# Performance work log

Measured on AMD Instinct MI355X. Metric: run time of the kernel, lower is better.

Reference implementation:

```python
import jax, jax.numpy as jnp
import numpy as np
import math

SUB_LEN = 5

def _row_mask(index, sub_len, win_len):
    # Faithful port of logsparseAttention.row_mask (numpy, built at trace time).
    log_l = math.ceil(math.log2(sub_len))
    mask = np.zeros(win_len, dtype=np.float32)
    if (win_len // sub_len) * 2 * log_l > index:
        mask[: index + 1] = 1.0
    else:
        while index >= 0:
            if index - log_l + 1 < 0:
                mask[:index] = 1.0
                break
            mask[index - log_l + 1 : index + 1] = 1.0
            for i in range(log_l):
                new_index = index - log_l + 1 - 2 ** i
                if index - new_index <= sub_len and new_index >= 0:
                    mask[new_index] = 1.0
            index -= sub_len
    return mask

def _log_mask(win_len, sub_len):
    m = np.stack([_row_mask(i, sub_len, win_len) for i in range(win_len)])
    return m[None, None]  # [1, 1, L, L]

def setup_inputs() -> dict:
    key = jax.random.key(0)
    kq, kk, kv = jax.random.split(key, 3)
    B, L, H, D = 4, 2048, 16, 64
    return {
        "queries": jax.random.normal(kq, (B, L, H, D), dtype=jnp.float32),
        "keys": jax.random.normal(kk, (B, L, H, D), dtype=jnp.float32),
        "values": jax.random.normal(kv, (B, L, H, D), dtype=jnp.float32),
        "attn_mask": jnp.zeros((1,), dtype=jnp.int32),  # unused by the module
    }

def reference(queries, keys, values, attn_mask):
    L = queries.shape[1]
    mask = jnp.asarray(_log_mask(L, SUB_LEN), dtype=queries.dtype)  # [1,1,L,L]
    q = jnp.swapaxes(queries, 1, 2)            # [B, H, L, D]
    k = jnp.transpose(keys, (0, 2, 3, 1))      # [B, H, D, L]
    v = jnp.swapaxes(values, 1, 2)             # [B, H, L, D]
    pre_att = jnp.matmul(q, k)                 # [B, H, L, L] (no scaling: scale=None)
    pre_att = pre_att * mask + (-1e9) * (1.0 - mask)
    att = jax.nn.softmax(pre_att, axis=-1)
    return jnp.matmul(att, v)                  # [B, H, L, D]
```

## Files before the change

### kernel.cpp

```cpp
#include <hip/hip_runtime.h>


typedef __attribute__((ext_vector_type(8))) short short8;
typedef __attribute__((ext_vector_type(4))) float floatx4;
typedef __attribute__((ext_vector_type(16))) float floatx16;
typedef _Float16 half8 __attribute__((ext_vector_type(8)));
typedef _Float16 half4 __attribute__((ext_vector_type(4)));
typedef unsigned int uint32_t4 __attribute__((ext_vector_type(4)));

#define NB 4
#define NL 2048
#define NH 16
#define ND 64
#define PADK 72
#define LOG2E 1.44269504088896340736f

#define KSW(row, col8) (((row) << 6) + ((col8) ^ (((row) & 7) << 3)))

static __device__ __forceinline__ unsigned short f2bf(float f) {
    unsigned int u = __float_as_uint(f);
    u += 0x7fff + ((u >> 16) & 1);
    return (unsigned short)(u >> 16);
}
static __device__ __forceinline__ float bf2f(unsigned short h) {
    return __uint_as_float(((unsigned int)h) << 16);
}
static __device__ __forceinline__ floatx16 fzero16() {
    floatx16 z;
    #pragma unroll
    for (int i = 0; i < 16; ++i) z[i] = 0.f;
    return z;
}

static __device__ __forceinline__ void plswap2(unsigned int& a, unsigned int& b, int hi) {
#if __has_builtin(__builtin_amdgcn_permlane32_swap)
    auto r = __builtin_amdgcn_permlane32_swap(a, b, false, false);
    a = (unsigned int)r[0];
    b = (unsigned int)r[1];
#else
    const unsigned int ax = (unsigned int)__shfl_xor((int)a, 32);
    const unsigned int bx = (unsigned int)__shfl_xor((int)b, 32);
    const unsigned int na = hi ? bx : a;
    const unsigned int nb = hi ? b  : ax;
    a = na; b = nb;
#endif
}
static __device__ __forceinline__ float xhalf_max(float v, int hi) {
    unsigned int a = __float_as_uint(v), b = __float_as_uint(v);
    plswap2(a, b, hi);
    return fmaxf(__uint_as_float(a), __uint_as_float(b));
}
static __device__ __forceinline__ float xhalf_sum(float v, int hi) {
    unsigned int a = __float_as_uint(v), b = __float_as_uint(v);
    plswap2(a, b, hi);
    return __uint_as_float(a) + __uint_as_float(b);
}

static __device__ __forceinline__ void pack_P(const floatx16& p, int hi, half8& pfa, half8& pfb) {
    unsigned int A0 = __builtin_bit_cast(unsigned int, __builtin_amdgcn_cvt_pkrtz(p[0],  p[1]));
    unsigned int B0 = __builtin_bit_cast(unsigned int, __builtin_amdgcn_cvt_pkrtz(p[2],  p[3]));
    unsigned int A1 = __builtin_bit_cast(unsigned int, __builtin_amdgcn_cvt_pkrtz(p[4],  p[5]));
    unsigned int B1 = __builtin_bit_cast(unsigned int, __builtin_amdgcn_cvt_pkrtz(p[6],  p[7]));
    unsigned int A2 = __builtin_bit_cast(unsigned int, __builtin_amdgcn_cvt_pkrtz(p[8],  p[9]));
    unsigned int B2 = __builtin_bit_cast(unsigned int, __builtin_amdgcn_cvt_pkrtz(p[10], p[11]));
    unsigned int A3 = __builtin_bit_cast(unsigned int, __builtin_amdgcn_cvt_pkrtz(p[12], p[13]));
    unsigned int B3 = __builtin_bit_cast(unsigned int, __builtin_amdgcn_cvt_pkrtz(p[14], p[15]));
    plswap2(A0, A1, hi); plswap2(B0, B1, hi);
    plswap2(A2, A3, hi); plswap2(B2, B3, hi);
    uint32_t4 wa = {A0, B0, A1, B1};
    uint32_t4 wb = {A2, B2, A3, B3};
    pfa = __builtin_bit_cast(half8, wa);
    pfb = __builtin_bit_cast(half8, wb);
}

__global__ __launch_bounds__(256)
void conv_kv(const float* __restrict__ Kg, const float* __restrict__ Vg,
             _Float16* __restrict__ Kf, _Float16* __restrict__ Vt) {
    __shared__ float tile[64][65];
    const int kt = blockIdx.x;
    const int bh = blockIdx.y;
    const int b  = bh >> 4, h = bh & 15;
    const int t  = threadIdx.x;
    const int row = t >> 2;
    const int seg = (t & 3) * 16;
    const size_t gsrc = (((size_t)(b * NL + kt * 64 + row) * NH + h) << 6) + seg;
    {
        float kv[16];
        #pragma unroll
        for (int i = 0; i < 16; i += 4) *(float4*)(kv + i) = *(const float4*)(Kg + gsrc + i);
        half8 o0, o1;
        #pragma unroll
        for (int j2 = 0; j2 < 8; ++j2) {
            o0[j2] = (_Float16)(kv[j2] * LOG2E);
            o1[j2] = (_Float16)(kv[8 + j2] * LOG2E);
        }
        _Float16* kd = Kf + (((size_t)(bh * NL + kt * 64 + row)) << 6) + seg;
        *(half8*)kd = o0;
        *(half8*)(kd + 8) = o1;
    }
    {
        #pragma unroll
        for (int i = 0; i < 16; i += 4) {
            float4 v = *(const float4*)(Vg + gsrc + i);
            tile[row][seg + i + 0] = v.x;
            tile[row][seg + i + 1] = v.y;
            tile[row][seg + i + 2] = v.z;
            tile[row][seg + i + 3] = v.w;
        }
    }
    __syncthreads();
    #pragma unroll
    for (int pass = 0; pass < 2; ++pass) {
        const int d  = pass * 32 + (t >> 3);
        const int kk = (t & 7) * 8;
        half8 o;
        #pragma unroll
        for (int j2 = 0; j2 < 8; ++j2) o[j2] = (_Float16)tile[kk + j2][d];
        *(half8*)(Vt + (((size_t)(bh * 64 + d)) << 11) + kt * 64 + kk) = o;
    }
}

__global__ __launch_bounds__(256, 4)
void lsattn_main(const float* __restrict__ Qg,
                 const _Float16* __restrict__ Kf,
                 const _Float16* __restrict__ Vt,
                 float* __restrict__ Og) {
    __shared__ alignas(16) _Float16 Ks[2][64 * 64];
    __shared__ alignas(16) _Float16 Vs[2][64 * 64];

    const int id   = (int)blockIdx.x;
    const int bh   = id & 63;
    const int pr   = id >> 6;
    const int tid  = threadIdx.x;
    const int lane = tid & 63;
    const int w    = tid >> 6;
    const int wq   = w & 1;
    const int lq   = lane & 31;
    const int hi   = lane >> 5;

    const int sa   = (w < 2) ? pr : 31 - pr;
    const int qrow = sa * 64 + wq * 32 + lq;
    const int TB   = 31 - pr;

    half8 qf[4];
    {
        const float* qp = Qg + (((size_t)((bh >> 4) * NL + qrow) * NH + (bh & 15)) << 6) + hi * 8;
        #pragma unroll
        for (int c = 0; c < 4; ++c) {
            float4 a = *(const float4*)(qp + c * 16);
            float4 b = *(const float4*)(qp + c * 16 + 4);
            qf[c][0] = (_Float16)a.x; qf[c][1] = (_Float16)a.y;
            qf[c][2] = (_Float16)a.z; qf[c][3] = (_Float16)a.w;
            qf[c][4] = (_Float16)b.x; qf[c][5] = (_Float16)b.y;
            qf[c][6] = (_Float16)b.z; qf[c][7] = (_Float16)b.w;
        }
    }

    floatx16 o0 = fzero16(), o1 = fzero16();
    float m_run = -1e30f, l_run = 0.f;

    const int srow = tid >> 3;
    const int sseg = (tid & 7) * 8;
    const _Float16* kgb = Kf + ((size_t)bh * NL + srow) * 64 + sseg;
    const _Float16* vgb = Vt + ((size_t)bh << 17) + (size_t)srow * NL + sseg;

    auto process_tile = [&](int t, const _Float16* Ksb, const _Float16* Vsb) {
        const bool diag  = (t == sa);
        const bool skip1 = diag && (wq == 0);

        floatx16 s0 = fzero16(), s1 = fzero16();
        __builtin_amdgcn_s_setprio(1);
        #pragma unroll
        for (int c = 0; c < 4; ++c) {
            half8 kf = *(const half8*)(Ksb + KSW(lq, c * 16 + hi * 8));
            s0 = __builtin_amdgcn_mfma_f32_32x32x16_f16(kf, qf[c], s0, 0, 0, 0);
        }
        if (!skip1) {
            #pragma unroll
            for (int c = 0; c < 4; ++c) {
                half8 kf = *(const half8*)(Ksb + KSW(32 + lq, c * 16 + hi * 8));
                s1 = __builtin_amdgcn_mfma_f32_32x32x16_f16(kf, qf[c], s1, 0, 0, 0);
            }
        }
        __builtin_amdgcn_s_setprio(0);

        if (diag) {
            if (wq == 0) {
                #pragma unroll
                for (int reg = 0; reg < 16; ++reg) {
                    const int key = (reg & 3) + ((reg >> 2) << 3) + (hi << 2);
                    if (key > lq) s0[reg] = -1e30f;
                }
            } else {
                #pragma unroll
                for (int reg = 0; reg < 16; ++reg) {
                    const int key = (reg & 3) + ((reg >> 2) << 3) + (hi << 2);
                    if (key > lq) s1[reg] = -1e30f;
                }
            }
        }

        float m4[4];
        #pragma unroll
        for (int s = 0; s < 4; ++s)
            m4[s] = fmaxf(fmaxf(s0[4*s], s0[4*s+1]), fmaxf(s0[4*s+2], s0[4*s+3]));
        float mt = fmaxf(fmaxf(m4[0], m4[1]), fmaxf(m4[2], m4[3]));
        if (!skip1) {
            float n4[4];
            #pragma unroll
            for (int s = 0; s < 4; ++s)
                n4[s] = fmaxf(fmaxf(s1[4*s], s1[4*s+1]), fmaxf(s1[4*s+2], s1[4*s+3]));
            mt = fmaxf(mt, fmaxf(fmaxf(n4[0], n4[1]), fmaxf(n4[2], n4[3])));
        }
        mt = xhalf_max(mt, hi);

        if (__any(mt > m_run + 8.f)) {
            const float mn = fmaxf(m_run, mt);
            const float al = __builtin_amdgcn_exp2f(m_run - mn);
            #pragma unroll
            for (int i = 0; i < 16; ++i) { o0[i] *= al; o1[i] *= al; }
            l_run *= al;
            m_run = mn;
        }

        float ls;
        {
            #pragma unroll
            for (int i = 0; i < 16; ++i) s0[i] = __builtin_amdgcn_exp2f(s0[i] - m_run);
            float t4[4];
            #pragma unroll
            for (int s = 0; s < 4; ++s)
                t4[s] = (s0[4*s] + s0[4*s+1]) + (s0[4*s+2] + s0[4*s+3]);
            ls = (t4[0] + t4[1]) + (t4[2] + t4[3]);

            half8 pfa, pfb;
            pack_P(s0, hi, pfa, pfb);
            __builtin_amdgcn_s_setprio(1);
            #pragma unroll
            for (int c = 0; c < 2; ++c) {
                half8 pf  = (c == 0) ? pfa : pfb;
                half8 vf0 = *(const half8*)(Vsb + KSW(lq,      c * 16 + hi * 8));
                half8 vf1 = *(const half8*)(Vsb + KSW(32 + lq, c * 16 + hi * 8));
                o0 = __builtin_amdgcn_mfma_f32_32x32x16_f16(vf0, pf, o0, 0, 0, 0);
                o1 = __builtin_amdgcn_mfma_f32_32x32x16_f16(vf1, pf, o1, 0, 0, 0);
            }
            __builtin_amdgcn_s_setprio(0);
        }

        if (!skip1) {
            #pragma unroll
            for (int i = 0; i < 16; ++i) s1[i] = __builtin_amdgcn_exp2f(s1[i] - m_run);
            float u4[4];
            #pragma unroll
            for (int s = 0; s < 4; ++s)
                u4[s] = (s1[4*s] + s1[4*s+1]) + (s1[4*s+2] + s1[4*s+3]);
            ls += (u4[0] + u4[1]) + (u4[2] + u4[3]);

            half8 pfa, pfb;
            pack_P(s1, hi, pfa, pfb);
            __builtin_amdgcn_s_setprio(1);
            #pragma unroll
            for (int c = 2; c < 4; ++c) {
                half8 pf  = (c == 2) ? pfa : pfb;
                half8 vf0 = *(const half8*)(Vsb + KSW(lq,      c * 16 + hi * 8));
                half8 vf1 = *(const half8*)(Vsb + KSW(32 + lq, c * 16 + hi * 8));
                o0 = __builtin_amdgcn_mfma_f32_32x32x16_f16(vf0, pf, o0, 0, 0, 0);
                o1 = __builtin_amdgcn_mfma_f32_32x32x16_f16(vf1, pf, o1, 0, 0, 0);
            }
            __builtin_amdgcn_s_setprio(0);
        }
        l_run += xhalf_sum(ls, hi);
    };

    {
        half8 k0 = *(const half8*)(kgb);
        half8 k1 = *(const half8*)(kgb + 2048);
        half8 v0 = *(const half8*)(vgb);
        half8 v1 = *(const half8*)(vgb + 32 * NL);
        *(half8*)(Ks[0] + KSW(srow,      sseg)) = k0;
        *(half8*)(Ks[0] + KSW(srow + 32, sseg)) = k1;
        *(half8*)(Vs[0] + KSW(srow,      sseg)) = v0;
        *(half8*)(Vs[0] + KSW(srow + 32, sseg)) = v1;
    }
    half8 k0 = *(const half8*)(kgb + 4096);
    half8 k1 = *(const half8*)(kgb + 4096 + 2048);
    half8 v0 = *(const half8*)(vgb + 64);
    half8 v1 = *(const half8*)(vgb + 64 + 32 * NL);
    __syncthreads();

    int cur = 0;
    for (int t = 0; t <= TB; ++t) {
        if (t < TB) {
            _Float16* kd = Ks[cur ^ 1];
            _Float16* vd = Vs[cur ^ 1];
            *(half8*)(kd + KSW(srow,      sseg)) = k0;
            *(half8*)(kd + KSW(srow + 32, sseg)) = k1;
            *(half8*)(vd + KSW(srow,      sseg)) = v0;
            *(half8*)(vd + KSW(srow + 32, sseg)) = v1;
            if (t + 1 < TB) {
                k0 = *(const half8*)(kgb + (size_t)(t + 2) * 4096);
                k1 = *(const half8*)(kgb + (size_t)(t + 2) * 4096 + 2048);
                v0 = *(const half8*)(vgb + (t + 2) * 64);
                v1 = *(const half8*)(vgb + (t + 2) * 64 + 32 * NL);
            }
        }
        if (t <= sa) process_tile(t, Ks[cur], Vs[cur]);
        if (t < TB) __syncthreads();
        cur ^= 1;
    }

    const float inv = 1.f / l_run;
    float* op = Og + ((size_t)bh * NL + qrow) * ND;
    #pragma unroll
    for (int s = 0; s < 4; ++s) {
        float4 x, y;
        x.x = o0[s * 4 + 0] * inv; x.y = o0[s * 4 + 1] * inv;
        x.z = o0[s * 4 + 2] * inv; x.w = o0[s * 4 + 3] * inv;
        *(float4*)(op + s * 8 + hi * 4) = x;
        y.x = o1[s * 4 + 0] * inv; y.y = o1[s * 4 + 1] * inv;
        y.z = o1[s * 4 + 2] * inv; y.w = o1[s * 4 + 3] * inv;
        *(float4*)(op + 32 + s * 8 + hi * 4) = y;
    }
}

__global__ __launch_bounds__(256)
void lsattn_fb(const float* __restrict__ Qg,
               const float* __restrict__ Kg,
               const float* __restrict__ Vg,
               float* __restrict__ Og) {
    __shared__ alignas(16) unsigned short Kh[64 * PADK];
    __shared__ alignas(16) unsigned short Kl[64 * PADK];
    __shared__ alignas(16) unsigned short Vh[64 * PADK];

    const int qt   = 31 - (int)blockIdx.x;
    const int bh   = blockIdx.y;
    const int tid  = threadIdx.x;
    const int lane = tid & 63;
    const int w    = tid >> 6;
    const int col  = lane & 15;
    const int quad = lane >> 4;
    const int qrow = qt * 64 + w * 16 + col;

    short8 qhi[2], qlo[2];
    {
        const float* qp = Qg + ((bh >> 4) * NL + qrow) * (NH * ND) + (bh & 15) * ND + quad * 8;
        #pragma unroll
        for (int c = 0; c < 2; ++c) {
            float qv[8];
            *(float4*)(qv + 0) = *(const float4*)(qp + c * 32);
            *(float4*)(qv + 4) = *(const float4*)(qp + c * 32 + 4);
            #pragma unroll
            for (int j = 0; j < 8; ++j) {
                unsigned short h = f2bf(qv[j]);
                qhi[c][j] = (short)h;
                qlo[c][j] = (short)f2bf(qv[j] - bf2f(h));
            }
        }
    }
    floatx4 ofrag[4];
    #pragma unroll
    for (int i = 0; i < 4; ++i) ofrag[i] = floatx4{0.f, 0.f, 0.f, 0.f};
    float m_run = -1e30f, l_run = 0.f;
    const int skey  = tid >> 2;
    const int sdb   = (tid & 3) * 16;
    const int gbase = (bh >> 4) * NL * NH * ND + (bh & 15) * ND;

    for (int t = 0; t <= qt; ++t) {
        const int j0 = t * 64;
        __syncthreads();
        {
            const int gro = gbase + (j0 + skey) * (NH * ND) + sdb;
            float kv[16], vv[16];
            #pragma unroll
            for (int i = 0; i < 16; i += 4) {
                *(float4*)(kv + i) = *(const float4*)(Kg + gro + i);
                *(float4*)(vv + i) = *(const float4*)(Vg + gro + i);
            }
            short8 h0, h1, l0, l1;
            #pragma unroll
            for (int j = 0; j < 8; ++j) {
                unsigned short h = f2bf(kv[j]);
                h0[j] = (short)h; l0[j] = (short)f2bf(kv[j] - bf2f(h));
                unsigned short g = f2bf(kv[8 + j]);
                h1[j] = (short)g; l1[j] = (short)f2bf(kv[8 + j] - bf2f(g));
            }
            *(short8*)(Kh + skey * PADK + sdb)     = h0;
            *(short8*)(Kh + skey * PADK + sdb + 8) = h1;
            *(short8*)(Kl + skey * PADK + sdb)     = l0;
            *(short8*)(Kl + skey * PADK + sdb + 8) = l1;
            #pragma unroll
            for (int i = 0; i < 16; ++i) Vh[(sdb + i) * PADK + skey] = f2bf(vv[i]);
        }
        __syncthreads();

        floatx4 stf[4];
        #pragma unroll
        for (int f = 0; f < 4; ++f) {
            floatx4 acc = floatx4{0.f, 0.f, 0.f, 0.f};
            #pragma unroll
            for (int c = 0; c < 2; ++c) {
                short8 kh = *(const short8*)(Kh + (f * 16 + col) * PADK + c * 32 + quad * 8);
                short8 kl = *(const short8*)(Kl + (f * 16 + col) * PADK + c * 32 + quad * 8);
                acc = __builtin_amdgcn_mfma_f32_16x16x32_bf16(kh, qhi[c], acc, 0, 0, 0);
                acc = __builtin_amdgcn_mfma_f32_16x16x32_bf16(kl, qhi[c], acc, 0, 0, 0);
                acc = __builtin_amdgcn_mfma_f32_16x16x32_bf16(kh, qlo[c], acc, 0, 0, 0);
            }
            stf[f] = acc;
        }
        if (t == qt) {
            #pragma unroll
            for (int f = 0; f < 4; ++f)
                #pragma unroll
                for (int r = 0; r < 4; ++r) {
                    const int key = j0 + f * 16 + quad * 4 + r;
                    if (key > qrow) stf[f][r] = -1e30f;
                }
        }
        float mt = -1e30f;
        #pragma unroll
        for (int f = 0; f < 4; ++f)
            #pragma unroll
            for (int r = 0; r < 4; ++r) mt = fmaxf(mt, stf[f][r]);
        mt = fmaxf(mt, __shfl_xor(mt, 16));
        mt = fmaxf(mt, __shfl_xor(mt, 32));
        const float m_new = fmaxf(m_run, mt);
        const float alpha = __expf(m_run - m_new);
        float ls = 0.f;
        #pragma unroll
        for (int f = 0; f < 4; ++f)
            #pragma unroll
            for (int r = 0; r < 4; ++r) {
                const float p = __expf(stf[f][r] - m_new);
                stf[f][r] = p; ls += p;
            }
        ls += __shfl_xor(ls, 16);
        ls += __shfl_xor(ls, 32);
        l_run = l_run * alpha + ls;
        m_run = m_new;
        #pragma unroll
        for (int mc = 0; mc < 4; ++mc) ofrag[mc] *= alpha;

        short8 pfrag[2];
        #pragma unroll
        for (int kc = 0; kc < 2; ++kc) {
            #pragma unroll
            for (int jj = 0; jj < 8; ++jj) {
                const int r  = jj & 3;
                const int sq = (quad & 1) * 2 + (jj >> 2);
                const int sl = col + (sq << 4);
                const float va = __shfl(stf[kc * 2 + 0][r], sl);
                const float vb = __shfl(stf[kc * 2 + 1][r], sl);
                pfrag[kc][jj] = (short)f2bf((quad & 2) ? vb : va);
            }
        }
        #pragma unroll
        for (int mc = 0; mc < 4; ++mc) {
            #pragma unroll
            for (int kc = 0; kc < 2; ++kc) {
                short8 vf = *(const short8*)(Vh + (mc * 16 + col) * PADK + kc * 32 + quad * 8);
                ofrag[mc] = __builtin_amdgcn_mfma_f32_16x16x32_bf16(vf, pfrag[kc], ofrag[mc], 0, 0, 0);
            }
        }
    }
    const float inv = 1.f / l_run;
    float* op = Og + ((size_t)bh * NL + qrow) * ND;
    #pragma unroll
    for (int mc = 0; mc < 4; ++mc) {
        float4 o;
        o.x = ofrag[mc][0] * inv; o.y = ofrag[mc][1] * inv;
        o.z = ofrag[mc][2] * inv; o.w = ofrag[mc][3] * inv;
        *(float4*)(op + mc * 16 + quad * 4) = o;
    }
}

extern "C" void kernel_launch(void* const* d_in, const int* in_sizes, int n_in,
                              void* d_out, int out_size, void* d_ws, size_t ws_size,
                              hipStream_t stream) {
    const float* Q = (const float*)d_in[0];
    const float* K = (const float*)d_in[1];
    const float* V = (const float*)d_in[2];
    float* O = (float*)d_out;

    const size_t elems = (size_t)NB * NL * NH * ND;
    if (ws_size >= 2 * elems * sizeof(_Float16)) {
        _Float16* Kf = (_Float16*)d_ws;
        _Float16* Vt = Kf + elems;
        conv_kv<<<dim3(32, 64), dim3(256), 0, stream>>>(K, V, Kf, Vt);
        lsattn_main<<<dim3(1024), dim3(256), 0, stream>>>(Q, Kf, Vt, O);
    } else {
        lsattn_fb<<<dim3(32, 64), dim3(256), 0, stream>>>(Q, K, V, O);
    }
}
```

Baseline: 207.4 us.

## Stage K/V tiles via direct global-to-LDS loads instead of register staging

Replaces the register-staged double buffer (global load to registers, then LDS store) with global_load_lds direct transfers. The swizzle moves into the global source addressing so each lane's 16-byte chunk lands in the swizzled LDS slot. The aim is to free VGPRs and drop the LDS write instructions. In exchange, every iteration now waits for all outstanding vector-memory operations before the barrier, which may expose load latency. Correctness depends on the per-wave 512-element contiguous LDS layout matching the KSW swizzle.

Measured after the change: 192.9 us. 7.0% less time.

```diff
diff --git a/kernel.cpp b/kernel.cpp
--- a/kernel.cpp
+++ b/kernel.cpp
@@ -30,6 +30,22 @@
     #pragma unroll
     for (int i = 0; i < 16; ++i) z[i] = 0.f;
     return z;
+}
+
+static __device__ __forceinline__ void drain_vmem() {
+    asm volatile("s_waitcnt vmcnt(0)" ::: "memory");
+    __builtin_amdgcn_sched_barrier(0);
+}
+
+static __device__ __forceinline__ void gload16(const _Float16* g, _Float16* l, int lane) {
+#if __has_builtin(__builtin_amdgcn_global_load_lds)
+    __builtin_amdgcn_global_load_lds(
+        (const __attribute__((address_space(1))) void*)g,
+        (__attribute__((address_space(3))) void*)l,
+        16, 0, 0);
+#else
+    *(half8*)(l + lane * 8) = *(const half8*)g;
+#endif
 }
 
 static __device__ __forceinline__ void plswap2(unsigned int& a, unsigned int& b, int hi) {
@@ -160,9 +176,20 @@
     float m_run = -1e30f, l_run = 0.f;
 
     const int srow = tid >> 3;
-    const int sseg = (tid & 7) * 8;
-    const _Float16* kgb = Kf + ((size_t)bh * NL + srow) * 64 + sseg;
-    const _Float16* vgb = Vt + ((size_t)bh << 17) + (size_t)srow * NL + sseg;
+    const int sseg = ((tid & 7) ^ ((tid >> 3) & 7)) * 8;
+    const _Float16* kg = Kf + ((size_t)bh * NL + srow) * 64 + sseg;
+    const _Float16* vg = Vt + ((size_t)bh << 17) + (size_t)srow * NL + sseg;
+
+    auto stage = [&](int t, int buf) {
+        _Float16* kb = (buf ? (_Float16*)Ks[1] : (_Float16*)Ks[0]) + w * 512;
+        _Float16* vb = (buf ? (_Float16*)Vs[1] : (_Float16*)Vs[0]) + w * 512;
+        const _Float16* ksrc = kg + (size_t)t * 4096;
+        const _Float16* vsrc = vg + t * 64;
+        gload16(ksrc,         kb,        lane);
+        gload16(ksrc + 2048,  kb + 2048, lane);
+        gload16(vsrc,         vb,        lane);
+        gload16(vsrc + 65536, vb + 2048, lane);
+    };
 
     auto process_tile = [&](int t, const _Float16* Ksb, const _Float16* Vsb) {
         const bool diag  = (t == sa);
@@ -272,40 +299,20 @@
         l_run += xhalf_sum(ls, hi);
     };
 
-    {
-        half8 k0 = *(const half8*)(kgb);
-        half8 k1 = *(const half8*)(kgb + 2048);
-        half8 v0 = *(const half8*)(vgb);
-        half8 v1 = *(const half8*)(vgb + 32 * NL);
-        *(half8*)(Ks[0] + KSW(srow,      sseg)) = k0;
-        *(half8*)(Ks[0] + KSW(srow + 32, sseg)) = k1;
-        *(half8*)(Vs[0] + KSW(srow,      sseg)) = v0;
-        *(half8*)(Vs[0] + KSW(srow + 32, sseg)) = v1;
-    }
-    half8 k0 = *(const half8*)(kgb + 4096);
-    half8 k1 = *(const half8*)(kgb + 4096 + 2048);
-    half8 v0 = *(const half8*)(vgb + 64);
-    half8 v1 = *(const half8*)(vgb + 64 + 32 * NL);
+    stage(0, 0);
+    drain_vmem();
     __syncthreads();
 
     int cur = 0;
     for (int t = 0; t <= TB; ++t) {
+        const _Float16* kcb = cur ? (const _Float16*)Ks[1] : (const _Float16*)Ks[0];
+        const _Float16* vcb = cur ? (const _Float16*)Vs[1] : (const _Float16*)Vs[0];
+        if (t < TB) stage(t + 1, cur ^ 1);
+        if (t <= sa) process_tile(t, kcb, vcb);
         if (t < TB) {
-            _Float16* kd = Ks[cur ^ 1];
-            _Float16* vd = Vs[cur ^ 1];
-            *(half8*)(kd + KSW(srow,      sseg)) = k0;
-            *(half8*)(kd + KSW(srow + 32, sseg)) = k1;
-            *(half8*)(vd + KSW(srow,      sseg)) = v0;
-            *(half8*)(vd + KSW(srow + 32, sseg)) = v1;
-            if (t + 1 < TB) {
-                k0 = *(const half8*)(kgb + (size_t)(t + 2) * 4096);
-                k1 = *(const half8*)(kgb + (size_t)(t + 2) * 4096 + 2048);
-                v0 = *(const half8*)(vgb + (t + 2) * 64);
-                v1 = *(const half8*)(vgb + (t + 2) * 64 + 32 * NL);
-            }
-        }
-        if (t <= sa) process_tile(t, Ks[cur], Vs[cur]);
-        if (t < TB) __syncthreads();
+            drain_vmem();
+            __syncthreads();
+        }
         cur ^= 1;
     }
 
```

## Replace double-buffered LDS K/V tiles with single buffer and drop setprio hints

Applied to the files above, without the earlier changes.

Replaces the two-stage LDS double buffer for K and V with a single shared tile. Each iteration now does a barrier, a store of the register-prefetched tile and a second barrier, with the next tile's global loads issued in between. This halves LDS use per block, which could allow more resident blocks. In exchange it adds a second barrier per iteration and removes the overlap between LDS stores and MFMA compute. The s_setprio priority hints around the MFMA sections are also removed.

After: 202.8 us. 2.2% less time.

```diff
diff --git a/kernel.cpp b/kernel.cpp
--- a/kernel.cpp
+++ b/kernel.cpp
@@ -125,8 +125,8 @@
                  const _Float16* __restrict__ Kf,
                  const _Float16* __restrict__ Vt,
                  float* __restrict__ Og) {
-    __shared__ alignas(16) _Float16 Ks[2][64 * 64];
-    __shared__ alignas(16) _Float16 Vs[2][64 * 64];
+    __shared__ alignas(16) _Float16 Ks[64 * 64];
+    __shared__ alignas(16) _Float16 Vs[64 * 64];
 
     const int id   = (int)blockIdx.x;
     const int bh   = id & 63;
@@ -164,25 +164,23 @@
     const _Float16* kgb = Kf + ((size_t)bh * NL + srow) * 64 + sseg;
     const _Float16* vgb = Vt + ((size_t)bh << 17) + (size_t)srow * NL + sseg;
 
-    auto process_tile = [&](int t, const _Float16* Ksb, const _Float16* Vsb) {
+    auto process_tile = [&](int t) {
         const bool diag  = (t == sa);
         const bool skip1 = diag && (wq == 0);
 
         floatx16 s0 = fzero16(), s1 = fzero16();
-        __builtin_amdgcn_s_setprio(1);
         #pragma unroll
         for (int c = 0; c < 4; ++c) {
-            half8 kf = *(const half8*)(Ksb + KSW(lq, c * 16 + hi * 8));
+            half8 kf = *(const half8*)(Ks + KSW(lq, c * 16 + hi * 8));
             s0 = __builtin_amdgcn_mfma_f32_32x32x16_f16(kf, qf[c], s0, 0, 0, 0);
         }
         if (!skip1) {
             #pragma unroll
             for (int c = 0; c < 4; ++c) {
-                half8 kf = *(const half8*)(Ksb + KSW(32 + lq, c * 16 + hi * 8));
+                half8 kf = *(const half8*)(Ks + KSW(32 + lq, c * 16 + hi * 8));
                 s1 = __builtin_amdgcn_mfma_f32_32x32x16_f16(kf, qf[c], s1, 0, 0, 0);
             }
         }
-        __builtin_amdgcn_s_setprio(0);
 
         if (diag) {
             if (wq == 0) {
@@ -235,16 +233,14 @@
 
             half8 pfa, pfb;
             pack_P(s0, hi, pfa, pfb);
-            __builtin_amdgcn_s_setprio(1);
             #pragma unroll
             for (int c = 0; c < 2; ++c) {
                 half8 pf  = (c == 0) ? pfa : pfb;
-                half8 vf0 = *(const half8*)(Vsb + KSW(lq,      c * 16 + hi * 8));
-                half8 vf1 = *(const half8*)(Vsb + KSW(32 + lq, c * 16 + hi * 8));
+                half8 vf0 = *(const half8*)(Vs + KSW(lq,      c * 16 + hi * 8));
+                half8 vf1 = *(const half8*)(Vs + KSW(32 + lq, c * 16 + hi * 8));
                 o0 = __builtin_amdgcn_mfma_f32_32x32x16_f16(vf0, pf, o0, 0, 0, 0);
                 o1 = __builtin_amdgcn_mfma_f32_32x32x16_f16(vf1, pf, o1, 0, 0, 0);
             }
-            __builtin_amdgcn_s_setprio(0);
         }
 
         if (!skip1) {
@@ -258,55 +254,39 @@
 
             half8 pfa, pfb;
             pack_P(s1, hi, pfa, pfb);
-            __builtin_amdgcn_s_setprio(1);
             #pragma unroll
             for (int c = 2; c < 4; ++c) {
                 half8 pf  = (c == 2) ? pfa : pfb;
-                half8 vf0 = *(const half8*)(Vsb + KSW(lq,      c * 16 + hi * 8));
-                half8 vf1 = *(const half8*)(Vsb + KSW(32 + lq, c * 16 + hi * 8));
+                half8 vf0 = *(const half8*)(Vs + KSW(lq,      c * 16 + hi * 8));
+                half8 vf1 = *(const half8*)(Vs + KSW(32 + lq, c * 16 + hi * 8));
                 o0 = __builtin_amdgcn_mfma_f32_32x32x16_f16(vf0, pf, o0, 0, 0, 0);
                 o1 = __builtin_amdgcn_mfma_f32_32x32x16_f16(vf1, pf, o1, 0, 0, 0);
             }
-            __builtin_amdgcn_s_setprio(0);
         }
         l_run += xhalf_sum(ls, hi);
     };
 
-    {
-        half8 k0 = *(const half8*)(kgb);
-        half8 k1 = *(const half8*)(kgb + 2048);
-        half8 v0 = *(const half8*)(vgb);
-        half8 v1 = *(const half8*)(vgb + 32 * NL);
-        *(half8*)(Ks[0] + KSW(srow,      sseg)) = k0;
-        *(half8*)(Ks[0] + KSW(srow + 32, sseg)) = k1;
-        *(half8*)(Vs[0] + KSW(srow,      sseg)) = v0;
-        *(half8*)(Vs[0] + KSW(srow + 32, sseg)) = v1;
-    }
-    half8 k0 = *(const half8*)(kgb + 4096);
-    half8 k1 = *(const half8*)(kgb + 4096 + 2048);
-    half8 v0 = *(const half8*)(vgb + 64);
-    half8 v1 = *(const half8*)(vgb + 64 + 32 * NL);
-    __syncthreads();
-
-    int cur = 0;
+    half8 k0 = *(const half8*)(kgb);
+    half8 k1 = *(const half8*)(kgb + 2048);
+    half8 v0 = *(const half8*)(vgb);
+    half8 v1 = *(const half8*)(vgb + 32 * NL);
+
     for (int t = 0; t <= TB; ++t) {
+        __syncthreads();
+        *(half8*)(Ks + KSW(srow,      sseg)) = k0;
+        *(half8*)(Ks + KSW(srow + 32, sseg)) = k1;
+        *(half8*)(Vs + KSW(srow,      sseg)) = v0;
+        *(half8*)(Vs + KSW(srow + 32, sseg)) = v1;
         if (t < TB) {
-            _Float16* kd = Ks[cur ^ 1];
-            _Float16* vd = Vs[cur ^ 1];
-            *(half8*)(kd + KSW(srow,      sseg)) = k0;
-            *(half8*)(kd + KSW(srow + 32, sseg)) = k1;
-            *(half8*)(vd + KSW(srow,      sseg)) = v0;
-            *(half8*)(vd + KSW(srow + 32, sseg)) = v1;
-            if (t + 1 < TB) {
-                k0 = *(const half8*)(kgb + (size_t)(t + 2) * 4096);
-                k1 = *(const half8*)(kgb + (size_t)(t + 2) * 4096 + 2048);
-                v0 = *(const half8*)(vgb + (t + 2) * 64);
-                v1 = *(const half8*)(vgb + (t + 2) * 64 + 32 * NL);
-            }
-        }
-        if (t <= sa) process_tile(t, Ks[cur], Vs[cur]);
-        if (t < TB) __syncthreads();
-        cur ^= 1;
+            k0 = *(const half8*)(kgb + (size_t)(t + 1) * 4096);
+            k1 = *(const half8*)(kgb + (size_t)(t + 1) * 4096 + 2048);
+            v0 = *(const half8*)(vgb + (t + 1) * 64);
+            v1 = *(const half8*)(vgb + (t + 1) * 64 + 32 * NL);
+        }
+        __syncthreads();
+
+        if (t > sa) continue;
+        process_tile(t);
     }
 
     const float inv = 1.f / l_run;
```
